# Optimization experiments

Measured on AMD Instinct MI355X. Metric: run time of the kernel, lower is better.

## Reference

```python
import jax, jax.numpy as jnp
import numpy as np

N = 50000      # nodes
K = 15         # k_max candidate neighbors per node
D = 128        # node_dim
H = 64         # hidden_dim
K_MIN = 2.0
K_MAX = 15.0
TAU = 0.5      # edge_tau
LAM = 1.0      # selector_lambda


def setup_inputs() -> dict:
    key = jax.random.key(0)
    ks = jax.random.split(key, 16)
    x = jax.random.normal(ks[0], (N, D), dtype=jnp.float32)
    src = jax.random.randint(ks[1], (N * K,), 0, N)
    dst = jnp.repeat(jnp.arange(N), K)  # edges grouped by dst, as the module requires
    edge_index = jnp.stack([src, dst]).astype(jnp.int64)
    edge_dist = jax.random.uniform(ks[2], (N * K,), dtype=jnp.float32)

    def lin(k, fin, fout):
        return jax.random.normal(k, (fin, fout), dtype=jnp.float32) / np.sqrt(fin)

    EIN = 2 * D + 1  # edge MLP input: [x_dst, x_src, dist]
    return {
        "x": x, "edge_index": edge_index, "edge_dist": edge_dist,
        "ew1": lin(ks[3], EIN, H), "eb1": jnp.zeros((H,), jnp.float32),
        "ew2": lin(ks[4], H, H),   "eb2": jnp.zeros((H,), jnp.float32),
        "ew3": lin(ks[5], H, 1),   "eb3": jnp.zeros((1,), jnp.float32),
        "dw1": lin(ks[6], D + 1, H), "db1": jnp.zeros((H,), jnp.float32),
        "dw2": lin(ks[7], H, H),     "db2": jnp.zeros((H,), jnp.float32),
        "dw3": lin(ks[8], H, 1),     "db3": jnp.zeros((1,), jnp.float32),
    }


def reference(x, edge_index, edge_dist, ew1, eb1, ew2, eb2, ew3, eb3,
              dw1, db1, dw2, db2, dw3, db3):
    src_mat = edge_index[0].reshape(N, K)              # (N, K)
    x_src = x[src_mat]                                 # gather: (N, K, D)
    x_dst = jnp.broadcast_to(x[:, None, :], (N, K, D))
    edge_feat = jnp.concatenate([x_dst, x_src, edge_dist.reshape(N, K, 1)], axis=-1)

    # edge MLP -> logits (eval mode: no gumbel-logistic noise)
    h = jax.nn.relu(edge_feat @ ew1 + eb1)
    h = jax.nn.relu(h @ ew2 + eb2)
    edge_logits = (h @ ew3 + eb3)[..., 0]              # (N, K)
    edge_energy = jax.nn.sigmoid(edge_logits / TAU)

    # degree MLP -> continuous k per node
    degree_hint = edge_energy.sum(axis=1, keepdims=True)
    g = jax.nn.relu(jnp.concatenate([x, degree_hint], axis=1) @ dw1 + db1)
    g = jax.nn.relu(g @ dw2 + db2)
    k_raw = (g @ dw3 + db3)[:, 0]
    k_cont = K_MIN + (K_MAX - K_MIN) * jax.nn.sigmoid(k_raw)  # (N,)

    # per-node descending sort + straight-through top-k gate
    perm = jnp.argsort(-edge_energy, axis=1)
    energy_sorted = jnp.take_along_axis(edge_energy, perm, axis=1)
    ranks = jnp.arange(1, K + 1, dtype=x.dtype)[None, :]
    gate_soft = jax.nn.sigmoid((k_cont[:, None] - ranks) / LAM)
    k_int = jnp.clip(jnp.round(k_cont), K_MIN, K_MAX)
    gate_hard = (ranks <= k_int[:, None]).astype(gate_soft.dtype)
    gate = gate_soft + jax.lax.stop_gradient(gate_hard - gate_soft)

    gated_sorted = energy_sorted * gate
    inv_perm = jnp.argsort(perm, axis=1)               # undo the sort
    edge_gate = jnp.take_along_axis(gate, inv_perm, axis=1)
    edge_weight = jnp.take_along_axis(gated_sorted, inv_perm, axis=1)

    denom = jnp.maximum(edge_weight.sum(axis=1, keepdims=True), 1e-12)
    edge_weight = edge_weight / denom
    return (edge_weight.reshape(-1), edge_gate.reshape(-1),
            edge_energy.reshape(-1), k_cont)
```

## Files before the change

### kernel.cpp

```cpp
#include <hip/hip_runtime.h>
#include <cmath>

#define NN 50000
#define KK 15
#define DD 128
#define HH 64
#define NKE (NN * KK)

__global__ __launch_bounds__(256) void kP(const float* __restrict__ x,
                                          const float* __restrict__ ew1,
                                          const float* __restrict__ dw1,
                                          float* __restrict__ ws) {
    int lane = threadIdx.x & 63;
    int wv = __builtin_amdgcn_readfirstlane((int)(threadIdx.x >> 6));
    int seg = blockIdx.y;
    int rb = blockIdx.x * 32 + wv * 8;
    if (rb >= NN) return;
    const float* W = (seg == 0) ? ew1 : (seg == 1) ? (ew1 + 128 * HH) : dw1;
    const float* xw = x + (size_t)rb * DD;

    float acc[8];
#pragma unroll
    for (int r = 0; r < 8; ++r) acc[r] = 0.f;

#pragma unroll 1
    for (int i4 = 0; i4 < DD / 4; ++i4) {
        float xv[8][4];
#pragma unroll
        for (int r = 0; r < 8; ++r) {
            float4 v = *(const float4*)(xw + r * DD + i4 * 4);
            xv[r][0] = v.x; xv[r][1] = v.y; xv[r][2] = v.z; xv[r][3] = v.w;
        }
#pragma unroll
        for (int k = 0; k < 4; ++k) {
            float w = W[(i4 * 4 + k) * HH + lane];
#pragma unroll
            for (int r = 0; r < 8; ++r)
                acc[r] = fmaf(xv[r][k], w, acc[r]);
        }
    }
    float* o = ws + (size_t)seg * NN * HH + (size_t)rb * HH + lane;
#pragma unroll
    for (int r = 0; r < 8; ++r) o[r * HH] = acc[r];
}

__global__ __launch_bounds__(256, 1) void kE(const int* __restrict__ srcIdx,
                                             const float* __restrict__ dist,
                                             const float* __restrict__ ws,
                                             const float* __restrict__ ew1,
                                             const float* __restrict__ eb1,
                                             const float* __restrict__ ew2,
                                             const float* __restrict__ eb2,
                                             const float* __restrict__ ew3,
                                             const float* __restrict__ eb3,
                                             float* __restrict__ energy_out) {
    int t = blockIdx.x * 256 + threadIdx.x;
    int e0 = t * 2;
    if (e0 >= NKE) return;
    int s0 = srcIdx[e0], s1 = srcIdx[e0 + 1];
    int d0 = e0 / KK, d1 = (e0 + 1) / KK;
    float di0 = dist[e0], di1 = dist[e0 + 1];
    const float4* XA = (const float4*)ws;
    const float4* XB = (const float4*)(ws + (size_t)NN * HH);
    const float* w1l = ew1 + 2 * DD * HH;

    float acc0[HH], acc1[HH];
#pragma unroll
    for (int j = 0; j < HH; ++j) { acc0[j] = 0.f; acc1[j] = 0.f; }

#pragma unroll 1
    for (int i4 = 0; i4 < HH / 4; ++i4) {
        float4 a0 = XA[d0 * 16 + i4], b0 = XB[s0 * 16 + i4];
        float4 a1 = XA[d1 * 16 + i4], b1 = XB[s1 * 16 + i4];
        float av0[4] = {a0.x, a0.y, a0.z, a0.w};
        float bv0[4] = {b0.x, b0.y, b0.z, b0.w};
        float av1[4] = {a1.x, a1.y, a1.z, a1.w};
        float bv1[4] = {b1.x, b1.y, b1.z, b1.w};
        float h0[4], h1v[4];
#pragma unroll
        for (int k = 0; k < 4; ++k) {
            float wl = w1l[i4 * 4 + k];
            float bb = eb1[i4 * 4 + k];
            h0[k]  = fmaxf(av0[k] + bv0[k] + di0 * wl + bb, 0.f);
            h1v[k] = fmaxf(av1[k] + bv1[k] + di1 * wl + bb, 0.f);
        }
#pragma unroll
        for (int k = 0; k < 4; ++k) {
            const float* wr = ew2 + (i4 * 4 + k) * HH;
#pragma unroll
            for (int jj = 0; jj < 16; ++jj) {
                acc0[jj * 4 + 0] = fmaf(h0[k], wr[jj * 4 + 0], acc0[jj * 4 + 0]);
                acc0[jj * 4 + 1] = fmaf(h0[k], wr[jj * 4 + 1], acc0[jj * 4 + 1]);
                acc0[jj * 4 + 2] = fmaf(h0[k], wr[jj * 4 + 2], acc0[jj * 4 + 2]);
                acc0[jj * 4 + 3] = fmaf(h0[k], wr[jj * 4 + 3], acc0[jj * 4 + 3]);
                acc1[jj * 4 + 0] = fmaf(h1v[k], wr[jj * 4 + 0], acc1[jj * 4 + 0]);
                acc1[jj * 4 + 1] = fmaf(h1v[k], wr[jj * 4 + 1], acc1[jj * 4 + 1]);
                acc1[jj * 4 + 2] = fmaf(h1v[k], wr[jj * 4 + 2], acc1[jj * 4 + 2]);
                acc1[jj * 4 + 3] = fmaf(h1v[k], wr[jj * 4 + 3], acc1[jj * 4 + 3]);
            }
        }
    }
    float lg0 = eb3[0], lg1 = eb3[0];
#pragma unroll
    for (int j = 0; j < HH; ++j) {
        float b2 = eb2[j], w3 = ew3[j];
        lg0 = fmaf(fmaxf(acc0[j] + b2, 0.f), w3, lg0);
        lg1 = fmaf(fmaxf(acc1[j] + b2, 0.f), w3, lg1);
    }
    float2 en;
    en.x = 1.f / (1.f + expf(-2.f * lg0));
    en.y = 1.f / (1.f + expf(-2.f * lg1));
    *(float2*)(energy_out + e0) = en;
}

__global__ __launch_bounds__(128, 1) void kF(const float* __restrict__ ws,
                                             const float* __restrict__ dw1,
                                             const float* __restrict__ db1,
                                             const float* __restrict__ dw2,
                                             const float* __restrict__ db2,
                                             const float* __restrict__ dw3,
                                             const float* __restrict__ db3,
                                             float* __restrict__ out) {
    int n = blockIdx.x * 128 + threadIdx.x;
    if (n >= NN) return;
    const float* energy = out + 2 * (size_t)NKE;

    float ev[KK];
    float dh = 0.f;
#pragma unroll
    for (int j = 0; j < KK; ++j) {
        ev[j] = energy[(size_t)n * KK + j];
        dh += ev[j];
    }

    const float4* XC = (const float4*)(ws + 2 * (size_t)NN * HH);
    const float* w1l = dw1 + DD * HH;

    float acc[HH];
#pragma unroll
    for (int j = 0; j < HH; ++j) acc[j] = 0.f;

#pragma unroll 1
    for (int i4 = 0; i4 < HH / 4; ++i4) {
        float4 c = XC[n * 16 + i4];
        float cv[4] = {c.x, c.y, c.z, c.w};
#pragma unroll
        for (int k = 0; k < 4; ++k) {
            float g = fmaxf(cv[k] + dh * w1l[i4 * 4 + k] + db1[i4 * 4 + k], 0.f);
            const float* wr = dw2 + (i4 * 4 + k) * HH;
#pragma unroll
            for (int jj = 0; jj < 16; ++jj) {
                acc[jj * 4 + 0] = fmaf(g, wr[jj * 4 + 0], acc[jj * 4 + 0]);
                acc[jj * 4 + 1] = fmaf(g, wr[jj * 4 + 1], acc[jj * 4 + 1]);
                acc[jj * 4 + 2] = fmaf(g, wr[jj * 4 + 2], acc[jj * 4 + 2]);
                acc[jj * 4 + 3] = fmaf(g, wr[jj * 4 + 3], acc[jj * 4 + 3]);
            }
        }
    }
    float kraw = db3[0];
#pragma unroll
    for (int j = 0; j < HH; ++j)
        kraw = fmaf(fmaxf(acc[j] + db2[j], 0.f), dw3[j], kraw);

    float kcont = 2.f + 13.f / (1.f + expf(-kraw));
    out[3 * (size_t)NKE + n] = kcont;

    float se[16];
    int si[16];
#pragma unroll
    for (int j = 0; j < KK; ++j) { se[j] = ev[j]; si[j] = j; }
    se[15] = -1.f; si[15] = 15;

#pragma unroll
    for (int p = 1; p < 16; p <<= 1) {
#pragma unroll
        for (int k = p; k >= 1; k >>= 1) {
#pragma unroll
            for (int j = k & (p - 1); j + k < 16; j += 2 * k) {
#pragma unroll
                for (int i = 0; i < k; ++i) {
                    int a = i + j, b = i + j + k;
                    if (b < 16 && (a / (2 * p)) == (b / (2 * p))) {
                        bool sw = (se[b] > se[a]) ||
                                  (se[b] == se[a] && si[b] < si[a]);
                        float ea = sw ? se[b] : se[a];
                        float eb = sw ? se[a] : se[b];
                        int ia = sw ? si[b] : si[a];
                        int ib = sw ? si[a] : si[b];
                        se[a] = ea; se[b] = eb; si[a] = ia; si[b] = ib;
                    }
                }
            }
        }
    }

    float kint = rintf(kcont);
    kint = fminf(fmaxf(kint, 2.f), 15.f);

    float wsrt[KK];
    float denom = 0.f;
#pragma unroll
    for (int r = 0; r < KK; ++r) {
        float sel = ((float)(r + 1) <= kint) ? 1.f : 0.f;
        float wv = se[r] * sel;
        wsrt[r] = wv;
        denom += wv;
    }
    denom = fmaxf(denom, 1e-12f);

#pragma unroll
    for (int r = 0; r < KK; ++r) {
        float sel = ((float)(r + 1) <= kint) ? 1.f : 0.f;
        int j0 = si[r];
        out[(size_t)NKE + (size_t)n * KK + j0] = sel;
        out[(size_t)n * KK + j0] = wsrt[r] / denom;
    }
}

extern "C" void kernel_launch(void* const* d_in, const int* in_sizes, int n_in,
                              void* d_out, int out_size, void* d_ws, size_t ws_size,
                              hipStream_t stream) {
    const float* x   = (const float*)d_in[0];
    const int*   ei  = (const int*)d_in[1];
    const float* ed  = (const float*)d_in[2];
    const float* ew1 = (const float*)d_in[3];
    const float* eb1 = (const float*)d_in[4];
    const float* ew2 = (const float*)d_in[5];
    const float* eb2 = (const float*)d_in[6];
    const float* ew3 = (const float*)d_in[7];
    const float* eb3 = (const float*)d_in[8];
    const float* dw1 = (const float*)d_in[9];
    const float* db1 = (const float*)d_in[10];
    const float* dw2 = (const float*)d_in[11];
    const float* db2 = (const float*)d_in[12];
    const float* dw3 = (const float*)d_in[13];
    const float* db3 = (const float*)d_in[14];
    float* out = (float*)d_out;
    float* ws  = (float*)d_ws;

    hipLaunchKernelGGL(kP, dim3((NN + 31) / 32, 3), dim3(256), 0, stream,
                       x, ew1, dw1, ws);
    hipLaunchKernelGGL(kE, dim3((NKE / 2 + 255) / 256), dim3(256), 0, stream,
                       ei, ed, ws, ew1, eb1, ew2, eb2, ew3, eb3,
                       out + 2 * (size_t)NKE);
    hipLaunchKernelGGL(kF, dim3((NN + 127) / 128), dim3(128), 0, stream,
                       ws, dw1, db1, dw2, db2, dw3, db3, out);
}
```

Measured before the change: 325.2 us.

## Fuse projection segments with LDS-staged x, one edge per thread in edge MLP

The projection kernel now stages 32 rows of x in shared memory once and computes all three weight segments in one pass, instead of launching three grid segments that each reread x. The edge MLP kernel drops from two edges per thread with 128 accumulators to one edge per thread with 64 accumulators. Its launch bounds allow several blocks per CU for higher occupancy, and the next A/B float4 is software-prefetched while weights are read as float4. The degree kernel gets the same prefetch and float4 weight loads. The risk is less weight-load amortisation per edge in exchange for more waves hiding gather latency.

```diff
diff --git a/kernel.cpp b/kernel.cpp
--- a/kernel.cpp
+++ b/kernel.cpp
@@ -11,40 +11,79 @@
                                           const float* __restrict__ ew1,
                                           const float* __restrict__ dw1,
                                           float* __restrict__ ws) {
-    int lane = threadIdx.x & 63;
-    int wv = __builtin_amdgcn_readfirstlane((int)(threadIdx.x >> 6));
-    int seg = blockIdx.y;
-    int rb = blockIdx.x * 32 + wv * 8;
-    if (rb >= NN) return;
-    const float* W = (seg == 0) ? ew1 : (seg == 1) ? (ew1 + 128 * HH) : dw1;
-    const float* xw = x + (size_t)rb * DD;
-
-    float acc[8];
-#pragma unroll
-    for (int r = 0; r < 8; ++r) acc[r] = 0.f;
+    __shared__ float xs[32 * 128];
+    int tid = threadIdx.x;
+    int rb = blockIdx.x * 32;
+    int nrow = NN - rb; if (nrow > 32) nrow = 32;
+    {
+        const float4* xg = (const float4*)(x + (size_t)rb * DD);
+        float4* xs4 = (float4*)xs;
+        int nf4 = nrow * 32;
+#pragma unroll
+        for (int i = 0; i < 4; ++i) {
+            int fi = i * 256 + tid;
+            if (fi < nf4) xs4[fi] = xg[fi];
+        }
+    }
+    __syncthreads();
+
+    int lane = tid & 63;
+    int wv = tid >> 6;
+    int r0 = rb + wv * 8;
+    if (r0 >= NN) return;
+
+    const float* W0 = ew1;
+    const float* W1 = ew1 + DD * HH;
+    const float* W2 = dw1;
+
+    float a0[8], a1[8], a2[8];
+#pragma unroll
+    for (int r = 0; r < 8; ++r) { a0[r] = 0.f; a1[r] = 0.f; a2[r] = 0.f; }
 
 #pragma unroll 1
     for (int i4 = 0; i4 < DD / 4; ++i4) {
-        float xv[8][4];
+        float w00 = W0[(i4 * 4 + 0) * HH + lane];
+        float w01 = W0[(i4 * 4 + 1) * HH + lane];
+        float w02 = W0[(i4 * 4 + 2) * HH + lane];
+        float w03 = W0[(i4 * 4 + 3) * HH + lane];
+        float w10 = W1[(i4 * 4 + 0) * HH + lane];
+        float w11 = W1[(i4 * 4 + 1) * HH + lane];
+        float w12 = W1[(i4 * 4 + 2) * HH + lane];
+        float w13 = W1[(i4 * 4 + 3) * HH + lane];
+        float w20 = W2[(i4 * 4 + 0) * HH + lane];
+        float w21 = W2[(i4 * 4 + 1) * HH + lane];
+        float w22 = W2[(i4 * 4 + 2) * HH + lane];
+        float w23 = W2[(i4 * 4 + 3) * HH + lane];
 #pragma unroll
         for (int r = 0; r < 8; ++r) {
-            float4 v = *(const float4*)(xw + r * DD + i4 * 4);
-            xv[r][0] = v.x; xv[r][1] = v.y; xv[r][2] = v.z; xv[r][3] = v.w;
-        }
-#pragma unroll
-        for (int k = 0; k < 4; ++k) {
-            float w = W[(i4 * 4 + k) * HH + lane];
-#pragma unroll
-            for (int r = 0; r < 8; ++r)
-                acc[r] = fmaf(xv[r][k], w, acc[r]);
-        }
-    }
-    float* o = ws + (size_t)seg * NN * HH + (size_t)rb * HH + lane;
-#pragma unroll
-    for (int r = 0; r < 8; ++r) o[r * HH] = acc[r];
-}
-
-__global__ __launch_bounds__(256, 1) void kE(const int* __restrict__ srcIdx,
+            float4 xv = *(const float4*)&xs[(wv * 8 + r) * 128 + i4 * 4];
+            a0[r] = fmaf(xv.x, w00, a0[r]);
+            a0[r] = fmaf(xv.y, w01, a0[r]);
+            a0[r] = fmaf(xv.z, w02, a0[r]);
+            a0[r] = fmaf(xv.w, w03, a0[r]);
+            a1[r] = fmaf(xv.x, w10, a1[r]);
+            a1[r] = fmaf(xv.y, w11, a1[r]);
+            a1[r] = fmaf(xv.z, w12, a1[r]);
+            a1[r] = fmaf(xv.w, w13, a1[r]);
+            a2[r] = fmaf(xv.x, w20, a2[r]);
+            a2[r] = fmaf(xv.y, w21, a2[r]);
+            a2[r] = fmaf(xv.z, w22, a2[r]);
+            a2[r] = fmaf(xv.w, w23, a2[r]);
+        }
+    }
+    float* o0 = ws + (size_t)r0 * HH + lane;
+    float* o1 = ws + (size_t)NN * HH + (size_t)r0 * HH + lane;
+    float* o2 = ws + 2 * (size_t)NN * HH + (size_t)r0 * HH + lane;
+#pragma unroll
+    for (int r = 0; r < 8; ++r)
+        if (r0 + r < NN) {
+            o0[r * HH] = a0[r];
+            o1[r * HH] = a1[r];
+            o2[r * HH] = a2[r];
+        }
+}
+
+__global__ __launch_bounds__(128, 4) void kE(const int* __restrict__ srcIdx,
                                              const float* __restrict__ dist,
                                              const float* __restrict__ ws,
                                              const float* __restrict__ ew1,
@@ -54,63 +93,50 @@
                                              const float* __restrict__ ew3,
                                              const float* __restrict__ eb3,
                                              float* __restrict__ energy_out) {
-    int t = blockIdx.x * 256 + threadIdx.x;
-    int e0 = t * 2;
-    if (e0 >= NKE) return;
-    int s0 = srcIdx[e0], s1 = srcIdx[e0 + 1];
-    int d0 = e0 / KK, d1 = (e0 + 1) / KK;
-    float di0 = dist[e0], di1 = dist[e0 + 1];
-    const float4* XA = (const float4*)ws;
-    const float4* XB = (const float4*)(ws + (size_t)NN * HH);
+    int e = blockIdx.x * 128 + threadIdx.x;
+    if (e >= NKE) return;
+    int s = srcIdx[e];
+    int d = e / KK;
+    float dd = dist[e];
+    const float* A = ws + (size_t)d * HH;
+    const float* B = ws + (size_t)NN * HH + (size_t)s * HH;
     const float* w1l = ew1 + 2 * DD * HH;
 
-    float acc0[HH], acc1[HH];
-#pragma unroll
-    for (int j = 0; j < HH; ++j) { acc0[j] = 0.f; acc1[j] = 0.f; }
-
+    float acc[HH];
+#pragma unroll
+    for (int j = 0; j < HH; ++j) acc[j] = 0.f;
+
+    float4 a4 = *(const float4*)A;
+    float4 b4 = *(const float4*)B;
 #pragma unroll 1
     for (int i4 = 0; i4 < HH / 4; ++i4) {
-        float4 a0 = XA[d0 * 16 + i4], b0 = XB[s0 * 16 + i4];
-        float4 a1 = XA[d1 * 16 + i4], b1 = XB[s1 * 16 + i4];
-        float av0[4] = {a0.x, a0.y, a0.z, a0.w};
-        float bv0[4] = {b0.x, b0.y, b0.z, b0.w};
-        float av1[4] = {a1.x, a1.y, a1.z, a1.w};
-        float bv1[4] = {b1.x, b1.y, b1.z, b1.w};
-        float h0[4], h1v[4];
-#pragma unroll
-        for (int k = 0; k < 4; ++k) {
-            float wl = w1l[i4 * 4 + k];
-            float bb = eb1[i4 * 4 + k];
-            h0[k]  = fmaxf(av0[k] + bv0[k] + di0 * wl + bb, 0.f);
-            h1v[k] = fmaxf(av1[k] + bv1[k] + di1 * wl + bb, 0.f);
-        }
+        float4 a = a4, b = b4;
+        int nx = (i4 + 1 < HH / 4) ? (i4 + 1) : i4;
+        a4 = *(const float4*)(A + nx * 4);
+        b4 = *(const float4*)(B + nx * 4);
+        float h[4];
+        h[0] = fmaxf(a.x + b.x + dd * w1l[i4 * 4 + 0] + eb1[i4 * 4 + 0], 0.f);
+        h[1] = fmaxf(a.y + b.y + dd * w1l[i4 * 4 + 1] + eb1[i4 * 4 + 1], 0.f);
+        h[2] = fmaxf(a.z + b.z + dd * w1l[i4 * 4 + 2] + eb1[i4 * 4 + 2], 0.f);
+        h[3] = fmaxf(a.w + b.w + dd * w1l[i4 * 4 + 3] + eb1[i4 * 4 + 3], 0.f);
 #pragma unroll
         for (int k = 0; k < 4; ++k) {
             const float* wr = ew2 + (i4 * 4 + k) * HH;
 #pragma unroll
-            for (int jj = 0; jj < 16; ++jj) {
-                acc0[jj * 4 + 0] = fmaf(h0[k], wr[jj * 4 + 0], acc0[jj * 4 + 0]);
-                acc0[jj * 4 + 1] = fmaf(h0[k], wr[jj * 4 + 1], acc0[jj * 4 + 1]);
-                acc0[jj * 4 + 2] = fmaf(h0[k], wr[jj * 4 + 2], acc0[jj * 4 + 2]);
-                acc0[jj * 4 + 3] = fmaf(h0[k], wr[jj * 4 + 3], acc0[jj * 4 + 3]);
-                acc1[jj * 4 + 0] = fmaf(h1v[k], wr[jj * 4 + 0], acc1[jj * 4 + 0]);
-                acc1[jj * 4 + 1] = fmaf(h1v[k], wr[jj * 4 + 1], acc1[jj * 4 + 1]);
-                acc1[jj * 4 + 2] = fmaf(h1v[k], wr[jj * 4 + 2], acc1[jj * 4 + 2]);
-                acc1[jj * 4 + 3] = fmaf(h1v[k], wr[jj * 4 + 3], acc1[jj * 4 + 3]);
+            for (int j4 = 0; j4 < 16; ++j4) {
+                float4 w = *(const float4*)(wr + j4 * 4);
+                acc[j4 * 4 + 0] = fmaf(h[k], w.x, acc[j4 * 4 + 0]);
+                acc[j4 * 4 + 1] = fmaf(h[k], w.y, acc[j4 * 4 + 1]);
+                acc[j4 * 4 + 2] = fmaf(h[k], w.z, acc[j4 * 4 + 2]);
+                acc[j4 * 4 + 3] = fmaf(h[k], w.w, acc[j4 * 4 + 3]);
             }
         }
     }
-    float lg0 = eb3[0], lg1 = eb3[0];
-#pragma unroll
-    for (int j = 0; j < HH; ++j) {
-        float b2 = eb2[j], w3 = ew3[j];
-        lg0 = fmaf(fmaxf(acc0[j] + b2, 0.f), w3, lg0);
-        lg1 = fmaf(fmaxf(acc1[j] + b2, 0.f), w3, lg1);
-    }
-    float2 en;
-    en.x = 1.f / (1.f + expf(-2.f * lg0));
-    en.y = 1.f / (1.f + expf(-2.f * lg1));
-    *(float2*)(energy_out + e0) = en;
+    float lg = eb3[0];
+#pragma unroll
+    for (int j = 0; j < HH; ++j)
+        lg = fmaf(fmaxf(acc[j] + eb2[j], 0.f), ew3[j], lg);
+    energy_out[e] = 1.f / (1.f + expf(-2.f * lg));
 }
 
 __global__ __launch_bounds__(128, 1) void kF(const float* __restrict__ ws,
@@ -133,27 +159,32 @@
         dh += ev[j];
     }
 
-    const float4* XC = (const float4*)(ws + 2 * (size_t)NN * HH);
+    const float* XC = ws + 2 * (size_t)NN * HH + (size_t)n * HH;
     const float* w1l = dw1 + DD * HH;
 
     float acc[HH];
 #pragma unroll
     for (int j = 0; j < HH; ++j) acc[j] = 0.f;
 
+    float4 c4 = *(const float4*)XC;
 #pragma unroll 1
     for (int i4 = 0; i4 < HH / 4; ++i4) {
-        float4 c = XC[n * 16 + i4];
+        float4 c = c4;
+        int nx = (i4 + 1 < HH / 4) ? (i4 + 1) : i4;
+        c4 = *(const float4*)(XC + nx * 4);
         float cv[4] = {c.x, c.y, c.z, c.w};
 #pragma unroll
-        for (int k = 0; k < 4; ++k) {
-            float g = fmaxf(cv[k] + dh * w1l[i4 * 4 + k] + db1[i4 * 4 + k], 0.f);
-            const float* wr = dw2 + (i4 * 4 + k) * HH;
-#pragma unroll
-            for (int jj = 0; jj < 16; ++jj) {
-                acc[jj * 4 + 0] = fmaf(g, wr[jj * 4 + 0], acc[jj * 4 + 0]);
-                acc[jj * 4 + 1] = fmaf(g, wr[jj * 4 + 1], acc[jj * 4 + 1]);
-                acc[jj * 4 + 2] = fmaf(g, wr[jj * 4 + 2], acc[jj * 4 + 2]);
-                acc[jj * 4 + 3] = fmaf(g, wr[jj * 4 + 3], acc[jj * 4 + 3]);
+        for (int m = 0; m < 4; ++m) {
+            int k = i4 * 4 + m;
+            float g = fmaxf(cv[m] + dh * w1l[k] + db1[k], 0.f);
+            const float* wr = dw2 + k * HH;
+#pragma unroll
+            for (int j4 = 0; j4 < 16; ++j4) {
+                float4 w = *(const float4*)(wr + j4 * 4);
+                acc[j4 * 4 + 0] = fmaf(g, w.x, acc[j4 * 4 + 0]);
+                acc[j4 * 4 + 1] = fmaf(g, w.y, acc[j4 * 4 + 1]);
+                acc[j4 * 4 + 2] = fmaf(g, w.z, acc[j4 * 4 + 2]);
+                acc[j4 * 4 + 3] = fmaf(g, w.w, acc[j4 * 4 + 3]);
             }
         }
     }
@@ -202,9 +233,9 @@
 #pragma unroll
     for (int r = 0; r < KK; ++r) {
         float sel = ((float)(r + 1) <= kint) ? 1.f : 0.f;
-        float wv = se[r] * sel;
-        wsrt[r] = wv;
-        denom += wv;
+        float wvv = se[r] * sel;
+        wsrt[r] = wvv;
+        denom += wvv;
     }
     denom = fmaxf(denom, 1e-12f);
 
@@ -238,9 +269,9 @@
     float* out = (float*)d_out;
     float* ws  = (float*)d_ws;
 
-    hipLaunchKernelGGL(kP, dim3((NN + 31) / 32, 3), dim3(256), 0, stream,
+    hipLaunchKernelGGL(kP, dim3((NN + 31) / 32), dim3(256), 0, stream,
                        x, ew1, dw1, ws);
-    hipLaunchKernelGGL(kE, dim3((NKE / 2 + 255) / 256), dim3(256), 0, stream,
+    hipLaunchKernelGGL(kE, dim3((NKE + 127) / 128), dim3(128), 0, stream,
                        ei, ed, ws, ew1, eb1, ew2, eb2, ew3, eb3,
                        out + 2 * (size_t)NKE);
     hipLaunchKernelGGL(kF, dim3((NN + 127) / 128), dim3(128), 0, stream,
```

New measurement: 272.2 us. 16.3% less time.
